# Optimization experiments

Measured on AMD Instinct MI355X. Metric: run time of the kernel, lower is better.

The kernel has to match this reference:

```python
import jax, jax.numpy as jnp
import numpy as np

B = 256
MAXN = 1000
EPG = 7813
K, K1, K2 = 30, 3, 27


def setup_inputs():
    counts = np.where(np.arange(B) % 2 == 0, MAXN, 800).astype(np.int64)
    NT = int(counts.sum())  # 230400 nodes
    offsets = np.concatenate([[0], np.cumsum(counts)[:-1]]).astype(np.int64)
    batch = np.repeat(np.arange(B, dtype=np.int64), counts)
    rng = np.random.RandomState(0)
    E = B * EPG
    gid = np.repeat(np.arange(B), EPG)
    n = counts[gid]
    src = (rng.rand(E) * n).astype(np.int64)
    dst = (src + 1 + (rng.rand(E) * (n - 1)).astype(np.int64)) % n  # no self loops
    edge_index = np.stack([offsets[gid] + src, offsets[gid] + dst])
    key = jax.random.key(0)
    ks = jax.random.split(key, 8)
    def lin(k, fi, fo):
        return jax.random.normal(k, (fi, fo), jnp.float32) / np.sqrt(float(fi))
    return {
        'x': jax.random.normal(ks[0], (NT, 128), jnp.float32),
        'edge_index': jnp.asarray(edge_index),
        'batch': jnp.asarray(batch),
        'W1': lin(ks[1], 128, 64), 'b1': jnp.zeros(64, jnp.float32),
        'W2': lin(ks[2], 64, 64), 'b2': jnp.zeros(64, jnp.float32),
        'W3': lin(ks[3], 64, 64), 'b3': jnp.zeros(64, jnp.float32),
        'W4': lin(ks[4], 64, 1), 'b4': jnp.zeros(1, jnp.float32),
        'conv5_w': jax.random.normal(ks[5], (64, 1, 193), jnp.float32) / np.sqrt(193.0),
        'conv5_b': jnp.zeros(64, jnp.float32),
        'conv6_w': jax.random.normal(ks[6], (64, 64, 5), jnp.float32) / np.sqrt(320.0),
        'conv6_b': jnp.zeros(64, jnp.float32),
        'fc_w': lin(ks[7], 704, 1600), 'fc_b': jnp.zeros(1600, jnp.float32),
        'num_graphs': B,
        'max_num_nodes': MAXN,
    }


def _gcn(h_in, W, b, row, col, w_edge, self_w, N):
    h = h_in @ W
    agg = jax.ops.segment_sum(h[row] * w_edge[:, None], col, num_segments=N)
    return agg + self_w[:, None] * h + b


def _forward(x, edge_index, batch, W1, b1, W2, b2, W3, b3, W4, b4, conv5_w, conv5_b, conv6_w, conv6_b, fc_w, fc_b, num_graphs, max_num_nodes):
    N = x.shape[0]
    row, col = edge_index[0], edge_index[1]
    # GCN symmetric normalization with implicit self loops: deg = in-degree + 1
    deg = jax.ops.segment_sum(jnp.ones(row.shape[0], x.dtype), col, num_segments=N) + 1.0
    dis = jax.lax.rsqrt(deg)
    w_edge = dis[row] * dis[col]
    self_w = dis * dis
    x1 = jnp.tanh(_gcn(x, W1, b1, row, col, w_edge, self_w, N))
    x2 = jnp.tanh(_gcn(x1, W2, b2, row, col, w_edge, self_w, N))
    x3 = jnp.tanh(_gcn(x2, W3, b3, row, col, w_edge, self_w, N))
    x4 = jnp.tanh(_gcn(x3, W4, b4, row, col, w_edge, self_w, N))
    xc = jnp.concatenate([x1, x2, x3, x4], axis=-1)  # [N, 193]
    D = xc.shape[1]
    Bn, maxN = num_graphs, max_num_nodes
    # to_dense_batch with fill_value = min - 1
    num_nodes = jax.ops.segment_sum(jnp.ones(N, jnp.int32), batch, num_segments=Bn)
    cum = jnp.concatenate([jnp.zeros(1, jnp.int32), jnp.cumsum(num_nodes)])
    fill = xc.min() - 1.0
    idx = jnp.arange(N) - cum[batch] + batch.astype(jnp.int32) * maxN
    dense = jnp.full((Bn * maxN, D), fill, xc.dtype).at[idx].set(xc).reshape(Bn, maxN, D)
    # SortPooling: sort nodes per graph by last channel, descending
    order = jnp.argsort(-dense[:, :, -1], axis=-1)
    dense = jnp.take_along_axis(dense, order[:, :, None], axis=1)
    x_sort = dense[:, :K2]
    x_sort = jnp.where(x_sort == fill, 0.0, x_sort).reshape(Bn, K2 * D)
    # SimilarityPooling on residual nodes: sim[i] = sum_j ||x_i - x_j||^2 over first min(num_nodes, Nr) rows
    res = dense[:, K2:]  # [B, Nr, D]
    Nr = maxN - K2
    nv = jnp.minimum(num_nodes, Nr)
    mask = jnp.arange(Nr)[None, :] < nv[:, None]
    sq = jnp.sum(res * res, axis=-1)  # [B, Nr]
    Srow = jnp.sum(jnp.where(mask[:, :, None], res, 0.0), axis=1)  # [B, D]
    Tsum = jnp.sum(jnp.where(mask, sq, 0.0), axis=1)  # [B]
    nf = nv.astype(xc.dtype)
    sim = nf[:, None] * sq + Tsum[:, None] - 2.0 * jnp.einsum('bnd,bd->bn', res, Srow)
    sim = jnp.where(mask, sim, -jnp.inf)
    _, top = jax.lax.top_k(sim, K1)  # first K1 rows of the descending sort
    x_simi = jnp.take_along_axis(res, top[:, :, None], axis=1).reshape(Bn, K1 * D)
    pooled = jnp.concatenate([x_sort, x_simi], axis=1)  # [B, K*D] = [B, 5790]
    # 1D conv head
    h = pooled[:, None, :]
    h = jax.nn.relu(jax.lax.conv_general_dilated(h, conv5_w, (D,), 'VALID', dimension_numbers=('NCH', 'OIH', 'NCH')) + conv5_b[None, :, None])  # [B,64,30]
    h = h.reshape(Bn, 64, K // 2, 2).max(axis=-1)  # MaxPool1d(2,2) -> [B,64,15]
    h = jax.nn.relu(jax.lax.conv_general_dilated(h, conv6_w, (1,), 'VALID', dimension_numbers=('NCH', 'OIH', 'NCH')) + conv6_b[None, :, None])  # [B,64,11]
    h = h.reshape(Bn, -1)  # [B, 704]
    return jax.nn.relu(h @ fc_w + fc_b)  # dropout is identity in eval mode


def reference(x, edge_index, batch, W1, b1, W2, b2, W3, b3, W4, b4, conv5_w, conv5_b, conv6_w, conv6_b, fc_w, fc_b, num_graphs, max_num_nodes):
    return _forward(x, edge_index, batch, W1, b1, W2, b2, W3, b3, W4, b4, conv5_w, conv5_b, conv6_w, conv6_b, fc_w, fc_b, num_graphs, max_num_nodes)
```

## Files before the change

kernel.cpp:

```cpp
#include <hip/hip_runtime.h>
#include <float.h>
#include <limits.h>

static const int BG    = 256;
static const int SORTN = 1024;
static const int DF    = 193;
static const int K2C   = 27;
static const int K1C   = 3;
static const int NRESC = 973;
static const int PLEN  = 5790;
static const int GPARTS= 8;
static const int MAXE  = 8192;

#define DEV static __device__ __forceinline__

DEV float warp_sum64(float v){
#pragma unroll
  for (int o = 1; o < 64; o <<= 1) v += __shfl_xor(v, o);
  return v;
}
DEV float warp_min64(float v){
#pragma unroll
  for (int o = 1; o < 64; o <<= 1) v = fminf(v, __shfl_xor(v, o));
  return v;
}
DEV float feat_at(const float* __restrict__ x1, const float* __restrict__ x2,
                  const float* __restrict__ x3, const float* __restrict__ x4,
                  int node, int d){
  if (d < 64)  return x1[node*64 + d];
  if (d < 128) return x2[node*64 + (d-64)];
  if (d < 192) return x3[node*64 + (d-128)];
  return x4[node];
}
DEV int xcd_swizzle(int bid, int nwg){
  int q = nwg >> 3, r = nwg & 7;
  int x = bid & 7, i = bid >> 3;
  return ((x < r) ? x*(q+1) : r*(q+1) + (x-r)*q) + i;
}

__global__ __launch_bounds__(256) void k_bounds(const int* __restrict__ batch, int* __restrict__ goff, int NT){
  int i = blockIdx.x*256 + threadIdx.x;
  if (i < NT){
    if (i == 0 || batch[i] != batch[i-1]) goff[batch[i]] = i;
    if (i == NT-1) goff[BG] = NT;
  }
}
__global__ void k_gcount(const int* __restrict__ goff, int* __restrict__ gcount){
  int g = blockIdx.x*256 + threadIdx.x;
  if (g < BG) gcount[g] = goff[g+1] - goff[g];
}

__global__ __launch_bounds__(1024) void k_build(const int* __restrict__ rows, const int* __restrict__ cols,
                                                const int* __restrict__ gcount, const int* __restrict__ goff,
                                                float* __restrict__ dis, int* __restrict__ csr_off,
                                                int* __restrict__ csr_src, float* __restrict__ csr_w,
                                                int NT, int E, int epg){
  __shared__ int   lsrc[MAXE];
  __shared__ float lw[MAXE];
  __shared__ int   cnt[1024];
  __shared__ int   offl[1024];
  __shared__ int   cur[1024];
  __shared__ float disl[1024];
  __shared__ int   sm[1024];
  int g = blockIdx.x, tid = threadIdx.x;
  int n = gcount[g], base = goff[g];
  int ebase = g*epg;
  cnt[tid] = 0;
  __syncthreads();
  for (int i = tid; i < epg; i += 1024)
    atomicAdd(&cnt[cols[ebase+i] - base], 1);
  __syncthreads();
  if (tid < n){
    float d = 1.0f / sqrtf((float)cnt[tid] + 1.0f);
    disl[tid] = d;
    dis[base + tid] = d;
  }
  sm[tid] = cnt[tid]; __syncthreads();
  for (int o = 1; o < 1024; o <<= 1){
    int add = (tid >= o) ? sm[tid - o] : 0;
    __syncthreads(); sm[tid] += add; __syncthreads();
  }
  int excl = (tid > 0) ? sm[tid - 1] : 0;
  offl[tid] = excl; cur[tid] = excl;
  __syncthreads();
  if (tid < n) csr_off[base + tid] = ebase + offl[tid];
  if (g == BG - 1 && tid == 0) csr_off[NT] = E;
  for (int i = tid; i < epg; i += 1024){
    int r = rows[ebase + i], c = cols[ebase + i];
    float w = disl[r - base] * disl[c - base];
    int pos = atomicAdd(&cur[c - base], 1);
    lsrc[pos] = r;
    lw[pos]   = w;
  }
  __syncthreads();
  if (tid < n){
    int s0 = offl[tid];
    int s1 = (tid + 1 < n) ? offl[tid + 1] : epg;
    for (int i = s0 + 1; i < s1; i++){
      int ks = lsrc[i]; float kw = lw[i];
      int j = i - 1;
      while (j >= s0 && lsrc[j] > ks){ lsrc[j+1] = lsrc[j]; lw[j+1] = lw[j]; j--; }
      lsrc[j+1] = ks; lw[j+1] = kw;
    }
  }
  __syncthreads();
  for (int i = tid; i < epg; i += 1024){
    csr_src[ebase + i] = lsrc[i];
    csr_w[ebase + i]   = lw[i];
  }
}

template<int K>
__global__ __launch_bounds__(256) void k_gemm(const float* __restrict__ X, const float* __restrict__ W,
                                              float* __restrict__ H, int NT){
  const int BK = 32, KP = 36, NC = K/BK, TR = 128;
  __shared__ __align__(16) float xL[TR*KP];
  __shared__ __align__(16) float wL[BK*64];
  int tid = threadIdx.x;
  int rbase = blockIdx.x * TR;
  float4 px[4], pw[2];
  auto pre = [&](int c){
    int k0 = c*BK;
#pragma unroll
    for (int q = 0; q < 4; q++){
      int p = q*256 + tid;
      int row = p >> 3, c4 = p & 7;
      int gr = rbase + row;
      float4 v = make_float4(0.f,0.f,0.f,0.f);
      if (gr < NT) v = *((const float4*)&X[(size_t)gr*K + k0 + c4*4]);
      px[q] = v;
    }
#pragma unroll
    for (int j = 0; j < 2; j++){
      int i = tid*2 + j;
      int kr = i >> 4, cc = (i & 15)*4;
      pw[j] = *((const float4*)&W[(size_t)(k0 + kr)*64 + cc]);
    }
  };
  pre(0);
  int r0 = tid >> 3;
  int cg = (tid & 7) * 8;
  float acc[4][8];
#pragma unroll
  for (int i = 0; i < 4; i++)
#pragma unroll
    for (int j = 0; j < 8; j++) acc[i][j] = 0.f;
  for (int c = 0; c < NC; c++){
    if (c > 0) __syncthreads();
#pragma unroll
    for (int q = 0; q < 4; q++){
      int p = q*256 + tid;
      int row = p >> 3, c4 = p & 7;
      *((float4*)&xL[row*KP + c4*4]) = px[q];
    }
#pragma unroll
    for (int j = 0; j < 2; j++){
      int i = tid*2 + j;
      int kr = i >> 4, cc = (i & 15)*4;
      *((float4*)&wL[kr*64 + cc]) = pw[j];
    }
    if (c + 1 < NC) pre(c + 1);
    __syncthreads();
    for (int kq = 0; kq < BK; kq += 4){
      float4 xr[4];
#pragma unroll
      for (int i = 0; i < 4; i++) xr[i] = *((const float4*)&xL[(r0 + 32*i)*KP + kq]);
#pragma unroll
      for (int kk = 0; kk < 4; kk++){
        float4 wa = *((const float4*)&wL[(kq+kk)*64 + cg]);
        float4 wb = *((const float4*)&wL[(kq+kk)*64 + cg + 4]);
#pragma unroll
        for (int i = 0; i < 4; i++){
          float xv = (kk==0)?xr[i].x:(kk==1)?xr[i].y:(kk==2)?xr[i].z:xr[i].w;
          acc[i][0] = fmaf(xv, wa.x, acc[i][0]);
          acc[i][1] = fmaf(xv, wa.y, acc[i][1]);
          acc[i][2] = fmaf(xv, wa.z, acc[i][2]);
          acc[i][3] = fmaf(xv, wa.w, acc[i][3]);
          acc[i][4] = fmaf(xv, wb.x, acc[i][4]);
          acc[i][5] = fmaf(xv, wb.y, acc[i][5]);
          acc[i][6] = fmaf(xv, wb.z, acc[i][6]);
          acc[i][7] = fmaf(xv, wb.w, acc[i][7]);
        }
      }
    }
  }
#pragma unroll
  for (int i = 0; i < 4; i++){
    int gr = rbase + r0 + 32*i;
    if (gr < NT){
      float4 oa = make_float4(acc[i][0], acc[i][1], acc[i][2], acc[i][3]);
      float4 ob = make_float4(acc[i][4], acc[i][5], acc[i][6], acc[i][7]);
      *((float4*)&H[(size_t)gr*64 + cg])     = oa;
      *((float4*)&H[(size_t)gr*64 + cg + 4]) = ob;
    }
  }
}

template<bool FUSE_DOT>
__global__ __launch_bounds__(256) void k_agg(const float* __restrict__ H, const int* __restrict__ off,
                                             const int* __restrict__ srcs, const float* __restrict__ ws,
                                             const float* __restrict__ dis, const float* __restrict__ bias,
                                             const float* __restrict__ W4, float* __restrict__ Xout,
                                             float* __restrict__ H4, int NT, int nwg){
  int sbid = xcd_swizzle(blockIdx.x, nwg);
  int wid_v = sbid*4 + (threadIdx.x >> 6);
  int lane  = threadIdx.x & 63;
  if (wid_v >= NT) return;
  int wid = __builtin_amdgcn_readfirstlane(wid_v);
  int s0 = off[wid], s1 = off[wid+1];
  float a0=0.f,a1=0.f,a2=0.f,a3=0.f,a4=0.f,a5=0.f,a6=0.f,a7=0.f;
  int e = s0;
  for (; e + 8 <= s1; e += 8){
    int   i0=srcs[e],  i1=srcs[e+1], i2=srcs[e+2], i3=srcs[e+3];
    int   i4=srcs[e+4],i5=srcs[e+5], i6=srcs[e+6], i7=srcs[e+7];
    float w0=ws[e],  w1=ws[e+1], w2=ws[e+2], w3=ws[e+3];
    float w4=ws[e+4],w5=ws[e+5], w6=ws[e+6], w7=ws[e+7];
    a0 = fmaf(w0, H[(size_t)i0*64 + lane], a0);
    a1 = fmaf(w1, H[(size_t)i1*64 + lane], a1);
    a2 = fmaf(w2, H[(size_t)i2*64 + lane], a2);
    a3 = fmaf(w3, H[(size_t)i3*64 + lane], a3);
    a4 = fmaf(w4, H[(size_t)i4*64 + lane], a4);
    a5 = fmaf(w5, H[(size_t)i5*64 + lane], a5);
    a6 = fmaf(w6, H[(size_t)i6*64 + lane], a6);
    a7 = fmaf(w7, H[(size_t)i7*64 + lane], a7);
  }
  if (e + 4 <= s1){
    int   i0=srcs[e],  i1=srcs[e+1], i2=srcs[e+2], i3=srcs[e+3];
    float w0=ws[e],  w1=ws[e+1], w2=ws[e+2], w3=ws[e+3];
    a0 = fmaf(w0, H[(size_t)i0*64 + lane], a0);
    a1 = fmaf(w1, H[(size_t)i1*64 + lane], a1);
    a2 = fmaf(w2, H[(size_t)i2*64 + lane], a2);
    a3 = fmaf(w3, H[(size_t)i3*64 + lane], a3);
    e += 4;
  }
  if (e     < s1) a4 = fmaf(ws[e],   H[(size_t)srcs[e]*64   + lane], a4);
  if (e + 1 < s1) a5 = fmaf(ws[e+1], H[(size_t)srcs[e+1]*64 + lane], a5);
  if (e + 2 < s1) a6 = fmaf(ws[e+2], H[(size_t)srcs[e+2]*64 + lane], a6);
  float acc = ((a0 + a1) + (a2 + a3)) + ((a4 + a5) + (a6 + a7));
  float dv = dis[wid];
  float out = acc + dv*dv*H[(size_t)wid*64 + lane] + bias[lane];
  float t = tanhf(out);
  Xout[(size_t)wid*64 + lane] = t;
  if (FUSE_DOT){
    float p = warp_sum64(t * W4[lane]);
    if (lane == 0) H4[wid] = p;
  }
}

__global__ __launch_bounds__(256) void k_agg1(const float* __restrict__ H4, const int* __restrict__ off,
                                              const int* __restrict__ srcs, const float* __restrict__ ws,
                                              const float* __restrict__ dis, const float* __restrict__ b4,
                                              float* __restrict__ x4, int NT){
  int v = blockIdx.x*256 + threadIdx.x;
  if (v >= NT) return;
  int s0 = off[v], s1 = off[v+1];
  float acc = 0.f;
  for (int e = s0; e < s1; e++) acc = fmaf(ws[e], H4[srcs[e]], acc);
  float dv = dis[v];
  x4[v] = tanhf(acc + dv*dv*H4[v] + b4[0]);
}

__global__ __launch_bounds__(256) void k_sq_min(const float* __restrict__ x1, const float* __restrict__ x2,
                                                const float* __restrict__ x3, const float* __restrict__ x4,
                                                int NT, float* __restrict__ sqv, float* __restrict__ bmin){
  int wid  = blockIdx.x*4 + (threadIdx.x >> 6);
  int lane = threadIdx.x & 63;
  float m = FLT_MAX;
  if (wid < NT){
    float a = x1[(size_t)wid*64 + lane];
    float b = x2[(size_t)wid*64 + lane];
    float c = x3[(size_t)wid*64 + lane];
    float s = a*a + b*b + c*c;
    m = fminf(fminf(a, b), c);
    float p = warp_sum64(s);
    if (lane == 0){
      float d = x4[wid];
      sqv[wid] = p + d*d;
      m = fminf(m, d);
    }
  }
  m = warp_min64(m);
  __shared__ float wm[4];
  if ((threadIdx.x & 63) == 0) wm[threadIdx.x >> 6] = m;
  __syncthreads();
  if (threadIdx.x == 0)
    bmin[blockIdx.x] = fminf(fminf(wm[0], wm[1]), fminf(wm[2], wm[3]));
}
__global__ __launch_bounds__(256) void k_min2(const float* __restrict__ bmin, int nb, float* __restrict__ minv){
  __shared__ float sm[256];
  float m = FLT_MAX;
  for (int i = threadIdx.x; i < nb; i += 256) m = fminf(m, bmin[i]);
  sm[threadIdx.x] = m; __syncthreads();
  for (int o = 128; o > 0; o >>= 1){
    if (threadIdx.x < o) sm[threadIdx.x] = fminf(sm[threadIdx.x], sm[threadIdx.x + o]);
    __syncthreads();
  }
  if (threadIdx.x == 0) minv[0] = sm[0];
}

__global__ __launch_bounds__(256) void k_gsum_part(const float* __restrict__ x1, const float* __restrict__ x2,
                                                   const float* __restrict__ x3, const float* __restrict__ x4,
                                                   const float* __restrict__ sqv, const int* __restrict__ gcount,
                                                   const int* __restrict__ goff, float* __restrict__ gpart){
  __shared__ float sm[256];
  int g = blockIdx.x, p = blockIdx.y, tid = threadIdx.x;
  int n = gcount[g]; size_t b64 = (size_t)goff[g] * 64;
  int tot = n * 64;
  int t0 = (int)(((long long)tot * p) / GPARTS);
  int t1 = (int)(((long long)tot * (p+1)) / GPARTS);
  float a1 = 0.f, a2 = 0.f, a3 = 0.f;
  for (int i = t0 + tid; i < t1; i += 256){
    a1 += x1[b64 + i];
    a2 += x2[b64 + i];
    a3 += x3[b64 + i];
  }
  float a4 = 0.f, asq = 0.f;
  int base = goff[g];
  int n0 = (int)(((long long)n * p) / GPARTS);
  int n1 = (int)(((long long)n * (p+1)) / GPARTS);
  for (int i = n0 + tid; i < n1; i += 256){
    a4  += x4[base + i];
    asq += sqv[base + i];
  }
  float* out = &gpart[(size_t)(g*GPARTS + p) * 194];
  sm[tid] = a1; __syncthreads();
  if (tid < 64) out[tid] = sm[tid] + sm[tid+64] + sm[tid+128] + sm[tid+192];
  __syncthreads();
  sm[tid] = a2; __syncthreads();
  if (tid < 64) out[64 + tid] = sm[tid] + sm[tid+64] + sm[tid+128] + sm[tid+192];
  __syncthreads();
  sm[tid] = a3; __syncthreads();
  if (tid < 64) out[128 + tid] = sm[tid] + sm[tid+64] + sm[tid+128] + sm[tid+192];
  __syncthreads();
  sm[tid] = a4; __syncthreads();
  for (int o = 128; o > 0; o >>= 1){
    if (tid < o) sm[tid] += sm[tid + o];
    __syncthreads();
  }
  if (tid == 0) out[192] = sm[0];
  __syncthreads();
  sm[tid] = asq; __syncthreads();
  for (int o = 128; o > 0; o >>= 1){
    if (tid < o) sm[tid] += sm[tid + o];
    __syncthreads();
  }
  if (tid == 0) out[193] = sm[0];
}
__global__ __launch_bounds__(256) void k_gcomb(const float* __restrict__ gpart, float* __restrict__ gstats){
  int g = blockIdx.x, c = threadIdx.x;
  if (c < 194){
    float s = 0.f;
    for (int p = 0; p < GPARTS; p++) s += gpart[(size_t)(g*GPARTS + p)*194 + c];
    gstats[g*194 + c] = s;
  }
}

__global__ __launch_bounds__(256) void k_sort(const float* __restrict__ x4, const int* __restrict__ gcount,
                                              const int* __restrict__ goff, int* __restrict__ sidxg,
                                              int* __restrict__ rank){
  __shared__ float sval[SORTN];
  __shared__ int   sidx[SORTN];
  int g = blockIdx.x, tid = threadIdx.x;
  int n = gcount[g], base = goff[g];
  for (int i = tid; i < SORTN; i += 256){
    sval[i] = (i < n) ? x4[base + i] : -FLT_MAX;
    sidx[i] = i;
  }
  __syncthreads();
  for (int k = 2; k <= SORTN; k <<= 1){
    for (int j = k >> 1; j > 0; j >>= 1){
      for (int t = tid; t < SORTN/2; t += 256){
        int i   = 2*t - (t & (j - 1));
        int ixj = i | j;
        bool up = ((i & k) == 0);
        float va = sval[i], vb = sval[ixj];
        int   ia = sidx[i], ib = sidx[ixj];
        bool aBeforeB = (va > vb) || (va == vb && ia < ib);
        bool bBeforeA = (vb > va) || (vb == va && ib < ia);
        bool doswap = up ? bBeforeA : aBeforeB;
        if (doswap){ sval[i] = vb; sval[ixj] = va; sidx[i] = ib; sidx[ixj] = ia; }
      }
      __syncthreads();
    }
  }
  for (int i = tid; i < SORTN; i += 256) sidxg[g*SORTN + i] = sidx[i];
  for (int i = tid; i < n; i += 256) rank[base + sidx[i]] = i;
}

__global__ __launch_bounds__(256) void k_top27(const float* __restrict__ x1, const float* __restrict__ x2,
                                               const float* __restrict__ x3, const float* __restrict__ x4,
                                               const float* __restrict__ sqv, const int* __restrict__ gcount,
                                               const int* __restrict__ goff, const int* __restrict__ sidxg,
                                               const float* __restrict__ gstats, const float* __restrict__ minv,
                                               float* __restrict__ Srow, float* __restrict__ TS,
                                               float* __restrict__ pooled){
  __shared__ int   t27n[K2C];
  __shared__ float srow_s[DF];
  int g = blockIdx.x, tid = threadIdx.x;
  int n = gcount[g], base = goff[g];
  float fill = minv[0] - 1.0f;
  int nv = (n < NRESC) ? n : NRESC;
  int nreal = n - K2C;
  int nfill = nv - nreal;
  if (tid < K2C) t27n[tid] = base + sidxg[g*SORTN + tid];
  __syncthreads();
  if (tid < DF){
    float s = 0.f;
    for (int r = 0; r < K2C; r++) s += feat_at(x1, x2, x3, x4, t27n[r], tid);
    float v = gstats[g*194 + tid] - s + (float)nfill * fill;
    srow_s[tid] = v;
    Srow[g*DF + tid] = v;
  }
  for (int i = tid; i < K2C*DF; i += 256){
    int r = i / DF, d = i - r*DF;
    pooled[(size_t)g*PLEN + i] = feat_at(x1, x2, x3, x4, t27n[r], d);
  }
  __syncthreads();
  if (tid == 0){
    float t27sq = 0.f;
    for (int r = 0; r < K2C; r++) t27sq += sqv[t27n[r]];
    float sqfill = (float)DF * fill * fill;
    float Tsum = gstats[g*194 + 193] - t27sq + (float)nfill * sqfill;
    float ssum = 0.f;
    for (int d = 0; d < DF; d++) ssum += srow_s[d];
    float nf = (float)nv;
    float simfill = nf * sqfill + Tsum - 2.0f * fill * ssum;
    TS[g*2 + 0] = Tsum;
    TS[g*2 + 1] = simfill;
  }
}

__global__ __launch_bounds__(256) void k_sim(const float* __restrict__ x1, const float* __restrict__ x2,
                                             const float* __restrict__ x3, const float* __restrict__ x4,
                                             const float* __restrict__ sqv, const int* __restrict__ batch,
                                             const int* __restrict__ gcount, const int* __restrict__ rank,
                                             const float* __restrict__ Srow, const float* __restrict__ TS,
                                             float* __restrict__ sim, int NT){
  int wid  = blockIdx.x*4 + (threadIdx.x >> 6);
  int lane = threadIdx.x & 63;
  if (wid >= NT) return;
  if (rank[wid] < K2C) return;
  int g = batch[wid];
  float a = x1[(size_t)wid*64 + lane];
  float b = x2[(size_t)wid*64 + lane];
  float c = x3[(size_t)wid*64 + lane];
  float s1 = Srow[g*DF + lane];
  float s2 = Srow[g*DF + 64 + lane];
  float s3 = Srow[g*DF + 128 + lane];
  float dot = warp_sum64(a*s1 + b*s2 + c*s3);
  if (lane == 0){
    float d = x4[wid];
    dot += d * Srow[g*DF + 192];
    int n = gcount[g];
    float nf = (float)((n < NRESC) ? n : NRESC);
    sim[wid] = nf * sqv[wid] + TS[g*2] - 2.0f * dot;
  }
}

DEV void top3_insert(float v, int j, float* tv, int* tj){
  if (v > tv[0] || (v == tv[0] && j < tj[0])){
    tv[2]=tv[1]; tj[2]=tj[1]; tv[1]=tv[0]; tj[1]=tj[0]; tv[0]=v; tj[0]=j;
  } else if (v > tv[1] || (v == tv[1] && j < tj[1])){
    tv[2]=tv[1]; tj[2]=tj[1]; tv[1]=v; tj[1]=j;
  } else if (v > tv[2] || (v == tv[2] && j < tj[2])){
    tv[2]=v; tj[2]=j;
  }
}
__global__ __launch_bounds__(256) void k_top3(const float* __restrict__ x1, const float* __restrict__ x2,
                                              const float* __restrict__ x3, const float* __restrict__ x4,
                                              const float* __restrict__ sim, const int* __restrict__ rank,
                                              const int* __restrict__ gcount, const int* __restrict__ goff,
                                              const int* __restrict__ sidxg, const float* __restrict__ TS,
                                              const float* __restrict__ minv, float* __restrict__ pooled){
  __shared__ float lv[256*3];
  __shared__ int   lj[256*3];
  __shared__ int   fsel[3];
  int g = blockIdx.x, tid = threadIdx.x;
  int n = gcount[g], base = goff[g];
  float fill = minv[0] - 1.0f;
  int nv = (n < NRESC) ? n : NRESC;
  int nreal = n - K2C;
  int nfill = nv - nreal;
  float tv[3] = {-FLT_MAX, -FLT_MAX, -FLT_MAX};
  int   tj[3] = {INT_MAX, INT_MAX, INT_MAX};
  for (int i = tid; i < n; i += 256){
    int node = base + i;
    int r = rank[node];
    if (r >= K2C) top3_insert(sim[node], r - K2C, tv, tj);
  }
#pragma unroll
  for (int q = 0; q < 3; q++){ lv[tid*3 + q] = tv[q]; lj[tid*3 + q] = tj[q]; }
  __syncthreads();
  for (int o = 128; o >= 1; o >>= 1){
    if (tid < o){
#pragma unroll
      for (int q = 0; q < 3; q++)
        top3_insert(lv[(tid + o)*3 + q], lj[(tid + o)*3 + q], tv, tj);
#pragma unroll
      for (int q = 0; q < 3; q++){ lv[tid*3 + q] = tv[q]; lj[tid*3 + q] = tj[q]; }
    }
    __syncthreads();
  }
  if (tid == 0){
    float simfill = TS[g*2 + 1];
    int ninj = (nfill < 3) ? nfill : 3;
    for (int q = 0; q < ninj; q++) top3_insert(simfill, nreal + q, tv, tj);
    fsel[0] = tj[0]; fsel[1] = tj[1]; fsel[2] = tj[2];
  }
  __syncthreads();
  for (int i = tid; i < K1C*DF; i += 256){
    int m = i / DF, d = i - m*DF;
    int j = fsel[m];
    float v;
    if (j < nreal){
      int node = base + sidxg[g*SORTN + K2C + j];
      v = feat_at(x1, x2, x3, x4, node, d);
    } else {
      v = fill;
    }
    pooled[(size_t)g*PLEN + K2C*DF + i] = v;
  }
}

__global__ __launch_bounds__(256) void k_head(const float* __restrict__ pooled, const float* __restrict__ w5,
                                              const float* __restrict__ b5, const float* __restrict__ w6,
                                              const float* __restrict__ b6, float* __restrict__ h6){
  __shared__ float smem[21760];
  float* pl  = smem;
  float* w5T = smem + 5790;
  float* h5  = smem + 18528;
  float* mx  = smem;
  float* w6T = smem + 960;
  int g = blockIdx.x, tid = threadIdx.x;
  for (int i = tid; i < PLEN; i += 256) pl[i] = pooled[(size_t)g*PLEN + i];
  for (int i = tid; i < 64*DF; i += 256){
    int o = i / DF, d = i - o*DF;
    w5T[d*66 + o] = w5[i];
  }
  __syncthreads();
  int o = tid & 63, tg = tid >> 6;
  for (int t = tg; t < 30; t += 4){
    const float* pr = &pl[t*DF];
    float a0=0.f, a1=0.f, a2=0.f, a3=0.f;
    for (int d = 0; d < 192; d += 4){
      a0 = fmaf(pr[d],   w5T[(d)*66 + o],   a0);
      a1 = fmaf(pr[d+1], w5T[(d+1)*66 + o], a1);
      a2 = fmaf(pr[d+2], w5T[(d+2)*66 + o], a2);
      a3 = fmaf(pr[d+3], w5T[(d+3)*66 + o], a3);
    }
    a0 = fmaf(pr[192], w5T[192*66 + o], a0);
    float acc = b5[o] + ((a0 + a1) + (a2 + a3));
    h5[t*64 + o] = fmaxf(acc, 0.f);
  }
  __syncthreads();
  for (int i = tid; i < 15*64; i += 256){
    int p = i >> 6, oo = i & 63;
    mx[i] = fmaxf(h5[(2*p)*64 + oo], h5[(2*p + 1)*64 + oo]);
  }
  __syncthreads();
  for (int i = tid; i < 64*64*5; i += 256){
    int oo = i / 320, rem = i - oo*320;
    w6T[rem*65 + oo] = w6[i];
  }
  __syncthreads();
  for (int t = tg; t < 11; t += 4){
    float a0=0.f, a1=0.f, a2=0.f, a3=0.f;
    for (int ii = 0; ii < 64; ii += 4){
#pragma unroll
      for (int k = 0; k < 5; k++){
        a0 = fmaf(mx[(t+k)*64 + ii],   w6T[((ii)*5   + k)*65 + o], a0);
        a1 = fmaf(mx[(t+k)*64 + ii+1], w6T[((ii+1)*5 + k)*65 + o], a1);
        a2 = fmaf(mx[(t+k)*64 + ii+2], w6T[((ii+2)*5 + k)*65 + o], a2);
        a3 = fmaf(mx[(t+k)*64 + ii+3], w6T[((ii+3)*5 + k)*65 + o], a3);
      }
    }
    float acc = b6[o] + ((a0 + a1) + (a2 + a3));
    h6[(size_t)g*704 + o*11 + t] = fmaxf(acc, 0.f);
  }
}

__global__ __launch_bounds__(256) void k_fc(const float* __restrict__ h6, const float* __restrict__ fw,
                                            const float* __restrict__ fb, float* __restrict__ out){
  int j  = blockIdx.x*64 + (threadIdx.x & 63);
  int b0 = __builtin_amdgcn_readfirstlane(blockIdx.y*16 + (threadIdx.x >> 6)*4);
  const float* h0p = h6 + (size_t)b0*704;
  const float* h1p = h0p + 704;
  const float* h2p = h0p + 1408;
  const float* h3p = h0p + 2112;
  float a0e=0.f,a0o=0.f,a1e=0.f,a1o=0.f,a2e=0.f,a2o=0.f,a3e=0.f,a3o=0.f;
#pragma unroll 4
  for (int k = 0; k < 704; k += 2){
    float w0 = fw[(size_t)k*1600 + j];
    float w1 = fw[(size_t)k*1600 + 1600 + j];
    a0e = fmaf(h0p[k], w0, a0e); a0o = fmaf(h0p[k+1], w1, a0o);
    a1e = fmaf(h1p[k], w0, a1e); a1o = fmaf(h1p[k+1], w1, a1o);
    a2e = fmaf(h2p[k], w0, a2e); a2o = fmaf(h2p[k+1], w1, a2o);
    a3e = fmaf(h3p[k], w0, a3e); a3o = fmaf(h3p[k+1], w1, a3o);
  }
  float fbj = fb[j];
  out[(size_t)b0*1600 + j]       = fmaxf(a0e + a0o + fbj, 0.f);
  out[(size_t)(b0+1)*1600 + j]   = fmaxf(a1e + a1o + fbj, 0.f);
  out[(size_t)(b0+2)*1600 + j]   = fmaxf(a2e + a2o + fbj, 0.f);
  out[(size_t)(b0+3)*1600 + j]   = fmaxf(a3e + a3o + fbj, 0.f);
}

extern "C" void kernel_launch(void* const* d_in, const int* in_sizes, int n_in,
                              void* d_out, int out_size, void* d_ws, size_t ws_size,
                              hipStream_t stream){
  const float* x    = (const float*)d_in[0];
  const int*   ei   = (const int*)d_in[1];
  const int*   batch= (const int*)d_in[2];
  const float* W1 = (const float*)d_in[3];  const float* b1 = (const float*)d_in[4];
  const float* W2 = (const float*)d_in[5];  const float* b2 = (const float*)d_in[6];
  const float* W3 = (const float*)d_in[7];  const float* b3 = (const float*)d_in[8];
  const float* W4 = (const float*)d_in[9];  const float* b4 = (const float*)d_in[10];
  const float* w5 = (const float*)d_in[11]; const float* b5 = (const float*)d_in[12];
  const float* w6 = (const float*)d_in[13]; const float* b6 = (const float*)d_in[14];
  const float* fw = (const float*)d_in[15]; const float* fb = (const float*)d_in[16];
  float* out = (float*)d_out;

  const int NT = in_sizes[2];
  const int E  = in_sizes[1] / 2;
  const int epg = E / BG;
  const int* rows = ei;
  const int* cols = ei + E;

  char* ws = (char*)d_ws;
  size_t off = 0;
  auto alloc = [&](size_t bytes) -> char* {
    off = (off + 255) & ~(size_t)255;
    char* p = ws + off;
    off += bytes;
    return p;
  };
  const int gridA  = (NT + 3) / 4;

  int*      gcount  = (int*)     alloc(BG * 4);
  int*      goff    = (int*)     alloc((BG + 1) * 4);
  float*    minv    = (float*)   alloc(4);
  float*    bmin    = (float*)   alloc((size_t)gridA * 4);
  float*    dis     = (float*)   alloc((size_t)NT * 4);
  int*      csr_off = (int*)     alloc((size_t)(NT + 1) * 4);
  int*      csr_src = (int*)     alloc((size_t)E * 4);
  float*    csr_w   = (float*)   alloc((size_t)E * 4);
  float*    Hbuf    = (float*)   alloc((size_t)NT * 64 * 4);
  float*    x1      = (float*)   alloc((size_t)NT * 64 * 4);
  float*    x2      = (float*)   alloc((size_t)NT * 64 * 4);
  float*    x3      = (float*)   alloc((size_t)NT * 64 * 4);
  float*    x4      = (float*)   alloc((size_t)NT * 4);
  float*    H4      = (float*)   alloc((size_t)NT * 4);
  float*    sqv     = (float*)   alloc((size_t)NT * 4);
  float*    simv    = (float*)   alloc((size_t)NT * 4);
  int*      rank    = (int*)     alloc((size_t)NT * 4);
  int*      sidxg   = (int*)     alloc((size_t)BG * SORTN * 4);
  float*    gpart   = (float*)   alloc((size_t)BG * GPARTS * 194 * 4);
  float*    gstats  = (float*)   alloc((size_t)BG * 194 * 4);
  float*    Srow    = (float*)   alloc((size_t)BG * DF * 4);
  float*    TS      = (float*)   alloc((size_t)BG * 2 * 4);
  float*    pooled  = (float*)   alloc((size_t)BG * PLEN * 4);
  float*    h6      = (float*)   alloc((size_t)BG * 704 * 4);

  const int gridNT = (NT + 255) / 256;

  k_bounds<<<gridNT, 256, 0, stream>>>(batch, goff, NT);
  k_gcount<<<1, 256, 0, stream>>>(goff, gcount);
  k_build<<<BG, 1024, 0, stream>>>(rows, cols, gcount, goff, dis, csr_off, csr_src, csr_w, NT, E, epg);

  const int gridG = (NT + 127) / 128;

  k_gemm<128><<<gridG, 256, 0, stream>>>(x, W1, Hbuf, NT);
  k_agg<false><<<gridA, 256, 0, stream>>>(Hbuf, csr_off, csr_src, csr_w, dis, b1, W4, x1, H4, NT, gridA);
  k_gemm<64><<<gridG, 256, 0, stream>>>(x1, W2, Hbuf, NT);
  k_agg<false><<<gridA, 256, 0, stream>>>(Hbuf, csr_off, csr_src, csr_w, dis, b2, W4, x2, H4, NT, gridA);
  k_gemm<64><<<gridG, 256, 0, stream>>>(x2, W3, Hbuf, NT);
  k_agg<true><<<gridA, 256, 0, stream>>>(Hbuf, csr_off, csr_src, csr_w, dis, b3, W4, x3, H4, NT, gridA);
  k_agg1<<<gridNT, 256, 0, stream>>>(H4, csr_off, csr_src, csr_w, dis, b4, x4, NT);

  k_sq_min<<<gridA, 256, 0, stream>>>(x1, x2, x3, x4, NT, sqv, bmin);
  k_min2<<<1, 256, 0, stream>>>(bmin, gridA, minv);
  k_gsum_part<<<dim3(BG, GPARTS), 256, 0, stream>>>(x1, x2, x3, x4, sqv, gcount, goff, gpart);
  k_gcomb<<<BG, 256, 0, stream>>>(gpart, gstats);
  k_sort<<<BG, 256, 0, stream>>>(x4, gcount, goff, sidxg, rank);
  k_top27<<<BG, 256, 0, stream>>>(x1, x2, x3, x4, sqv, gcount, goff, sidxg, gstats, minv, Srow, TS, pooled);
  k_sim<<<gridA, 256, 0, stream>>>(x1, x2, x3, x4, sqv, batch, gcount, rank, Srow, TS, simv, NT);
  k_top3<<<BG, 256, 0, stream>>>(x1, x2, x3, x4, simv, rank, gcount, goff, sidxg, TS, minv, pooled);

  k_head<<<BG, 256, 0, stream>>>(pooled, w5, b5, w6, b6, h6);
  k_fc<<<dim3(25, 16), 256, 0, stream>>>(h6, fw, fb, out);
}
```

Baseline: 722.7 us.

## Vectorize GCN aggregation to float4 per quarter-wave and fuse stats kernels

The aggregation kernel now has each 16-lane quarter of a wavefront handle one node with float4 gathers, so one wavefront processes four nodes instead of one. This cuts the number of gather instructions and raises memory-level parallelism. The separate square-norm/min kernel and the per-graph partial-sum kernel are merged into one per-graph stats kernel, so x1..x3 are read once instead of twice and a launch is removed. The merged kernel does a wave reduction per node, which adds shuffle work.

```diff
diff --git a/kernel.cpp b/kernel.cpp
--- a/kernel.cpp
+++ b/kernel.cpp
@@ -203,47 +203,84 @@
                                              const float* __restrict__ W4, float* __restrict__ Xout,
                                              float* __restrict__ H4, int NT, int nwg){
   int sbid = xcd_swizzle(blockIdx.x, nwg);
-  int wid_v = sbid*4 + (threadIdx.x >> 6);
-  int lane  = threadIdx.x & 63;
-  if (wid_v >= NT) return;
-  int wid = __builtin_amdgcn_readfirstlane(wid_v);
-  int s0 = off[wid], s1 = off[wid+1];
-  float a0=0.f,a1=0.f,a2=0.f,a3=0.f,a4=0.f,a5=0.f,a6=0.f,a7=0.f;
+  int wv   = threadIdx.x >> 6;
+  int lane = threadIdx.x & 63;
+  int sub  = lane >> 4;
+  int ql   = lane & 15;
+  int node = sbid*16 + wv*4 + sub;
+  if (node >= NT) return;
+  int s0 = off[node], s1 = off[node+1];
+  float4 a0=make_float4(0,0,0,0),a1=a0,a2=a0,a3=a0,a4=a0,a5=a0,a6=a0,a7=a0;
+  int cb = ql*4;
   int e = s0;
   for (; e + 8 <= s1; e += 8){
     int   i0=srcs[e],  i1=srcs[e+1], i2=srcs[e+2], i3=srcs[e+3];
     int   i4=srcs[e+4],i5=srcs[e+5], i6=srcs[e+6], i7=srcs[e+7];
     float w0=ws[e],  w1=ws[e+1], w2=ws[e+2], w3=ws[e+3];
     float w4=ws[e+4],w5=ws[e+5], w6=ws[e+6], w7=ws[e+7];
-    a0 = fmaf(w0, H[(size_t)i0*64 + lane], a0);
-    a1 = fmaf(w1, H[(size_t)i1*64 + lane], a1);
-    a2 = fmaf(w2, H[(size_t)i2*64 + lane], a2);
-    a3 = fmaf(w3, H[(size_t)i3*64 + lane], a3);
-    a4 = fmaf(w4, H[(size_t)i4*64 + lane], a4);
-    a5 = fmaf(w5, H[(size_t)i5*64 + lane], a5);
-    a6 = fmaf(w6, H[(size_t)i6*64 + lane], a6);
-    a7 = fmaf(w7, H[(size_t)i7*64 + lane], a7);
+    float4 h0=*((const float4*)&H[(size_t)i0*64+cb]);
+    float4 h1=*((const float4*)&H[(size_t)i1*64+cb]);
+    float4 h2=*((const float4*)&H[(size_t)i2*64+cb]);
+    float4 h3=*((const float4*)&H[(size_t)i3*64+cb]);
+    float4 h4=*((const float4*)&H[(size_t)i4*64+cb]);
+    float4 h5=*((const float4*)&H[(size_t)i5*64+cb]);
+    float4 h6=*((const float4*)&H[(size_t)i6*64+cb]);
+    float4 h7=*((const float4*)&H[(size_t)i7*64+cb]);
+    a0.x=fmaf(w0,h0.x,a0.x); a0.y=fmaf(w0,h0.y,a0.y); a0.z=fmaf(w0,h0.z,a0.z); a0.w=fmaf(w0,h0.w,a0.w);
+    a1.x=fmaf(w1,h1.x,a1.x); a1.y=fmaf(w1,h1.y,a1.y); a1.z=fmaf(w1,h1.z,a1.z); a1.w=fmaf(w1,h1.w,a1.w);
+    a2.x=fmaf(w2,h2.x,a2.x); a2.y=fmaf(w2,h2.y,a2.y); a2.z=fmaf(w2,h2.z,a2.z); a2.w=fmaf(w2,h2.w,a2.w);
+    a3.x=fmaf(w3,h3.x,a3.x); a3.y=fmaf(w3,h3.y,a3.y); a3.z=fmaf(w3,h3.z,a3.z); a3.w=fmaf(w3,h3.w,a3.w);
+    a4.x=fmaf(w4,h4.x,a4.x); a4.y=fmaf(w4,h4.y,a4.y); a4.z=fmaf(w4,h4.z,a4.z); a4.w=fmaf(w4,h4.w,a4.w);
+    a5.x=fmaf(w5,h5.x,a5.x); a5.y=fmaf(w5,h5.y,a5.y); a5.z=fmaf(w5,h5.z,a5.z); a5.w=fmaf(w5,h5.w,a5.w);
+    a6.x=fmaf(w6,h6.x,a6.x); a6.y=fmaf(w6,h6.y,a6.y); a6.z=fmaf(w6,h6.z,a6.z); a6.w=fmaf(w6,h6.w,a6.w);
+    a7.x=fmaf(w7,h7.x,a7.x); a7.y=fmaf(w7,h7.y,a7.y); a7.z=fmaf(w7,h7.z,a7.z); a7.w=fmaf(w7,h7.w,a7.w);
   }
   if (e + 4 <= s1){
     int   i0=srcs[e],  i1=srcs[e+1], i2=srcs[e+2], i3=srcs[e+3];
     float w0=ws[e],  w1=ws[e+1], w2=ws[e+2], w3=ws[e+3];
-    a0 = fmaf(w0, H[(size_t)i0*64 + lane], a0);
-    a1 = fmaf(w1, H[(size_t)i1*64 + lane], a1);
-    a2 = fmaf(w2, H[(size_t)i2*64 + lane], a2);
-    a3 = fmaf(w3, H[(size_t)i3*64 + lane], a3);
+    float4 h0=*((const float4*)&H[(size_t)i0*64+cb]);
+    float4 h1=*((const float4*)&H[(size_t)i1*64+cb]);
+    float4 h2=*((const float4*)&H[(size_t)i2*64+cb]);
+    float4 h3=*((const float4*)&H[(size_t)i3*64+cb]);
+    a0.x=fmaf(w0,h0.x,a0.x); a0.y=fmaf(w0,h0.y,a0.y); a0.z=fmaf(w0,h0.z,a0.z); a0.w=fmaf(w0,h0.w,a0.w);
+    a1.x=fmaf(w1,h1.x,a1.x); a1.y=fmaf(w1,h1.y,a1.y); a1.z=fmaf(w1,h1.z,a1.z); a1.w=fmaf(w1,h1.w,a1.w);
+    a2.x=fmaf(w2,h2.x,a2.x); a2.y=fmaf(w2,h2.y,a2.y); a2.z=fmaf(w2,h2.z,a2.z); a2.w=fmaf(w2,h2.w,a2.w);
+    a3.x=fmaf(w3,h3.x,a3.x); a3.y=fmaf(w3,h3.y,a3.y); a3.z=fmaf(w3,h3.z,a3.z); a3.w=fmaf(w3,h3.w,a3.w);
     e += 4;
   }
-  if (e     < s1) a4 = fmaf(ws[e],   H[(size_t)srcs[e]*64   + lane], a4);
-  if (e + 1 < s1) a5 = fmaf(ws[e+1], H[(size_t)srcs[e+1]*64 + lane], a5);
-  if (e + 2 < s1) a6 = fmaf(ws[e+2], H[(size_t)srcs[e+2]*64 + lane], a6);
-  float acc = ((a0 + a1) + (a2 + a3)) + ((a4 + a5) + (a6 + a7));
-  float dv = dis[wid];
-  float out = acc + dv*dv*H[(size_t)wid*64 + lane] + bias[lane];
-  float t = tanhf(out);
-  Xout[(size_t)wid*64 + lane] = t;
+  if (e < s1){
+    float w = ws[e]; float4 h=*((const float4*)&H[(size_t)srcs[e]*64+cb]);
+    a4.x=fmaf(w,h.x,a4.x); a4.y=fmaf(w,h.y,a4.y); a4.z=fmaf(w,h.z,a4.z); a4.w=fmaf(w,h.w,a4.w);
+  }
+  if (e + 1 < s1){
+    float w = ws[e+1]; float4 h=*((const float4*)&H[(size_t)srcs[e+1]*64+cb]);
+    a5.x=fmaf(w,h.x,a5.x); a5.y=fmaf(w,h.y,a5.y); a5.z=fmaf(w,h.z,a5.z); a5.w=fmaf(w,h.w,a5.w);
+  }
+  if (e + 2 < s1){
+    float w = ws[e+2]; float4 h=*((const float4*)&H[(size_t)srcs[e+2]*64+cb]);
+    a6.x=fmaf(w,h.x,a6.x); a6.y=fmaf(w,h.y,a6.y); a6.z=fmaf(w,h.z,a6.z); a6.w=fmaf(w,h.w,a6.w);
+  }
+  float4 acc;
+  acc.x = ((a0.x+a1.x)+(a2.x+a3.x)) + ((a4.x+a5.x)+(a6.x+a7.x));
+  acc.y = ((a0.y+a1.y)+(a2.y+a3.y)) + ((a4.y+a5.y)+(a6.y+a7.y));
+  acc.z = ((a0.z+a1.z)+(a2.z+a3.z)) + ((a4.z+a5.z)+(a6.z+a7.z));
+  acc.w = ((a0.w+a1.w)+(a2.w+a3.w)) + ((a4.w+a5.w)+(a6.w+a7.w));
+  float dv = dis[node];
+  float dv2 = dv*dv;
+  float4 hs = *((const float4*)&H[(size_t)node*64 + cb]);
+  float4 bb = *((const float4*)&bias[cb]);
+  float4 t;
+  t.x = tanhf(acc.x + dv2*hs.x + bb.x);
+  t.y = tanhf(acc.y + dv2*hs.y + bb.y);
+  t.z = tanhf(acc.z + dv2*hs.z + bb.z);
+  t.w = tanhf(acc.w + dv2*hs.w + bb.w);
+  *((float4*)&Xout[(size_t)node*64 + cb]) = t;
   if (FUSE_DOT){
-    float p = warp_sum64(t * W4[lane]);
-    if (lane == 0) H4[wid] = p;
+    float4 w4v = *((const float4*)&W4[cb]);
+    float p = t.x*w4v.x + t.y*w4v.y + t.z*w4v.z + t.w*w4v.w;
+#pragma unroll
+    for (int o = 1; o < 16; o <<= 1) p += __shfl_xor(p, o);
+    if (ql == 0) H4[node] = p;
   }
 }
 
@@ -260,31 +297,65 @@
   x4[v] = tanhf(acc + dv*dv*H4[v] + b4[0]);
 }
 
-__global__ __launch_bounds__(256) void k_sq_min(const float* __restrict__ x1, const float* __restrict__ x2,
-                                                const float* __restrict__ x3, const float* __restrict__ x4,
-                                                int NT, float* __restrict__ sqv, float* __restrict__ bmin){
-  int wid  = blockIdx.x*4 + (threadIdx.x >> 6);
-  int lane = threadIdx.x & 63;
-  float m = FLT_MAX;
-  if (wid < NT){
-    float a = x1[(size_t)wid*64 + lane];
-    float b = x2[(size_t)wid*64 + lane];
-    float c = x3[(size_t)wid*64 + lane];
-    float s = a*a + b*b + c*c;
-    m = fminf(fminf(a, b), c);
-    float p = warp_sum64(s);
+__global__ __launch_bounds__(256) void k_stats(const float* __restrict__ x1, const float* __restrict__ x2,
+                                               const float* __restrict__ x3, const float* __restrict__ x4,
+                                               const int* __restrict__ gcount, const int* __restrict__ goff,
+                                               float* __restrict__ sqv, float* __restrict__ gpart,
+                                               float* __restrict__ bmin){
+  __shared__ float sm[256];
+  __shared__ float wm[4];
+  int g = blockIdx.x, p = blockIdx.y, tid = threadIdx.x;
+  int wv = tid >> 6, lane = tid & 63;
+  int n = gcount[g], base = goff[g];
+  int n0 = (int)(((long long)n * p) / GPARTS);
+  int n1 = (int)(((long long)n * (p+1)) / GPARTS);
+  float a1 = 0.f, a2 = 0.f, a3 = 0.f;
+  float a4 = 0.f, asq = 0.f;
+  float mn = FLT_MAX;
+  for (int i = n0 + wv; i < n1; i += 4){
+    size_t node = (size_t)(base + i);
+    float v1 = x1[node*64 + lane];
+    float v2 = x2[node*64 + lane];
+    float v3 = x3[node*64 + lane];
+    a1 += v1; a2 += v2; a3 += v3;
+    mn = fminf(mn, fminf(fminf(v1, v2), v3));
+    float s = warp_sum64(v1*v1 + v2*v2 + v3*v3);
     if (lane == 0){
-      float d = x4[wid];
-      sqv[wid] = p + d*d;
-      m = fminf(m, d);
-    }
-  }
-  m = warp_min64(m);
-  __shared__ float wm[4];
-  if ((threadIdx.x & 63) == 0) wm[threadIdx.x >> 6] = m;
-  __syncthreads();
-  if (threadIdx.x == 0)
-    bmin[blockIdx.x] = fminf(fminf(wm[0], wm[1]), fminf(wm[2], wm[3]));
+      float d = x4[node];
+      float sq = s + d*d;
+      sqv[node] = sq;
+      a4 += d; asq += sq;
+      mn = fminf(mn, d);
+    }
+  }
+  float* out = &gpart[(size_t)(g*GPARTS + p) * 194];
+  sm[tid] = a1; __syncthreads();
+  if (tid < 64) out[tid] = sm[tid] + sm[tid+64] + sm[tid+128] + sm[tid+192];
+  __syncthreads();
+  sm[tid] = a2; __syncthreads();
+  if (tid < 64) out[64 + tid] = sm[tid] + sm[tid+64] + sm[tid+128] + sm[tid+192];
+  __syncthreads();
+  sm[tid] = a3; __syncthreads();
+  if (tid < 64) out[128 + tid] = sm[tid] + sm[tid+64] + sm[tid+128] + sm[tid+192];
+  __syncthreads();
+  sm[tid] = (lane == 0) ? a4 : 0.f; __syncthreads();
+  for (int o = 128; o > 0; o >>= 1){
+    if (tid < o) sm[tid] += sm[tid + o];
+    __syncthreads();
+  }
+  if (tid == 0) out[192] = sm[0];
+  __syncthreads();
+  sm[tid] = (lane == 0) ? asq : 0.f; __syncthreads();
+  for (int o = 128; o > 0; o >>= 1){
+    if (tid < o) sm[tid] += sm[tid + o];
+    __syncthreads();
+  }
+  if (tid == 0) out[193] = sm[0];
+  mn = warp_min64(mn);
+  if (lane == 0) wm[wv] = mn;
+  __syncthreads();
+  if (tid == 0)
+    bmin[g*GPARTS + p] = fminf(fminf(wm[0], wm[1]), fminf(wm[2], wm[3]));
 }
 __global__ __launch_bounds__(256) void k_min2(const float* __restrict__ bmin, int nb, float* __restrict__ minv){
   __shared__ float sm[256];
@@ -296,55 +367,6 @@
     __syncthreads();
   }
   if (threadIdx.x == 0) minv[0] = sm[0];
-}
-
-__global__ __launch_bounds__(256) void k_gsum_part(const float* __restrict__ x1, const float* __restrict__ x2,
-                                                   const float* __restrict__ x3, const float* __restrict__ x4,
-                                                   const float* __restrict__ sqv, const int* __restrict__ gcount,
-                                                   const int* __restrict__ goff, float* __restrict__ gpart){
-  __shared__ float sm[256];
-  int g = blockIdx.x, p = blockIdx.y, tid = threadIdx.x;
-  int n = gcount[g]; size_t b64 = (size_t)goff[g] * 64;
-  int tot = n * 64;
-  int t0 = (int)(((long long)tot * p) / GPARTS);
-  int t1 = (int)(((long long)tot * (p+1)) / GPARTS);
-  float a1 = 0.f, a2 = 0.f, a3 = 0.f;
-  for (int i = t0 + tid; i < t1; i += 256){
-    a1 += x1[b64 + i];
-    a2 += x2[b64 + i];
-    a3 += x3[b64 + i];
-  }
-  float a4 = 0.f, asq = 0.f;
-  int base = goff[g];
-  int n0 = (int)(((long long)n * p) / GPARTS);
-  int n1 = (int)(((long long)n * (p+1)) / GPARTS);
-  for (int i = n0 + tid; i < n1; i += 256){
-    a4  += x4[base + i];
-    asq += sqv[base + i];
-  }
-  float* out = &gpart[(size_t)(g*GPARTS + p) * 194];
-  sm[tid] = a1; __syncthreads();
-  if (tid < 64) out[tid] = sm[tid] + sm[tid+64] + sm[tid+128] + sm[tid+192];
-  __syncthreads();
-  sm[tid] = a2; __syncthreads();
-  if (tid < 64) out[64 + tid] = sm[tid] + sm[tid+64] + sm[tid+128] + sm[tid+192];
-  __syncthreads();
-  sm[tid] = a3; __syncthreads();
-  if (tid < 64) out[128 + tid] = sm[tid] + sm[tid+64] + sm[tid+128] + sm[tid+192];
-  __syncthreads();
-  sm[tid] = a4; __syncthreads();
-  for (int o = 128; o > 0; o >>= 1){
-    if (tid < o) sm[tid] += sm[tid + o];
-    __syncthreads();
-  }
-  if (tid == 0) out[192] = sm[0];
-  __syncthreads();
-  sm[tid] = asq; __syncthreads();
-  for (int o = 128; o > 0; o >>= 1){
-    if (tid < o) sm[tid] += sm[tid + o];
-    __syncthreads();
-  }
-  if (tid == 0) out[193] = sm[0];
 }
 __global__ __launch_bounds__(256) void k_gcomb(const float* __restrict__ gpart, float* __restrict__ gstats){
   int g = blockIdx.x, c = threadIdx.x;
@@ -633,12 +655,11 @@
     off += bytes;
     return p;
   };
-  const int gridA  = (NT + 3) / 4;
 
   int*      gcount  = (int*)     alloc(BG * 4);
   int*      goff    = (int*)     alloc((BG + 1) * 4);
   float*    minv    = (float*)   alloc(4);
-  float*    bmin    = (float*)   alloc((size_t)gridA * 4);
+  float*    bmin    = (float*)   alloc((size_t)BG * GPARTS * 4);
   float*    dis     = (float*)   alloc((size_t)NT * 4);
   int*      csr_off = (int*)     alloc((size_t)(NT + 1) * 4);
   int*      csr_src = (int*)     alloc((size_t)E * 4);
@@ -661,6 +682,8 @@
   float*    h6      = (float*)   alloc((size_t)BG * 704 * 4);
 
   const int gridNT = (NT + 255) / 256;
+  const int gridA  = (NT + 15) / 16;
+  const int gridS  = (NT + 3) / 4;
 
   k_bounds<<<gridNT, 256, 0, stream>>>(batch, goff, NT);
   k_gcount<<<1, 256, 0, stream>>>(goff, gcount);
@@ -676,13 +699,12 @@
   k_agg<true><<<gridA, 256, 0, stream>>>(Hbuf, csr_off, csr_src, csr_w, dis, b3, W4, x3, H4, NT, gridA);
   k_agg1<<<gridNT, 256, 0, stream>>>(H4, csr_off, csr_src, csr_w, dis, b4, x4, NT);
 
-  k_sq_min<<<gridA, 256, 0, stream>>>(x1, x2, x3, x4, NT, sqv, bmin);
-  k_min2<<<1, 256, 0, stream>>>(bmin, gridA, minv);
-  k_gsum_part<<<dim3(BG, GPARTS), 256, 0, stream>>>(x1, x2, x3, x4, sqv, gcount, goff, gpart);
+  k_stats<<<dim3(BG, GPARTS), 256, 0, stream>>>(x1, x2, x3, x4, gcount, goff, sqv, gpart, bmin);
+  k_min2<<<1, 256, 0, stream>>>(bmin, BG*GPARTS, minv);
   k_gcomb<<<BG, 256, 0, stream>>>(gpart, gstats);
   k_sort<<<BG, 256, 0, stream>>>(x4, gcount, goff, sidxg, rank);
   k_top27<<<BG, 256, 0, stream>>>(x1, x2, x3, x4, sqv, gcount, goff, sidxg, gstats, minv, Srow, TS, pooled);
-  k_sim<<<gridA, 256, 0, stream>>>(x1, x2, x3, x4, sqv, batch, gcount, rank, Srow, TS, simv, NT);
+  k_sim<<<gridS, 256, 0, stream>>>(x1, x2, x3, x4, sqv, batch, gcount, rank, Srow, TS, simv, NT);
   k_top3<<<BG, 256, 0, stream>>>(x1, x2, x3, x4, simv, rank, gcount, goff, sidxg, TS, minv, pooled);
 
   k_head<<<BG, 256, 0, stream>>>(pooled, w5, b5, w6, b6, h6);
```

After: 637.4 us. 1.13x faster.
